# Optimization experiments

Measured on AMD Instinct MI355X. Metric: run time of the kernel, lower is better.

Reference implementation:

```python
import jax, jax.numpy as jnp
import numpy as np

B, N, D, K = 16, 1024, 512, 8
NUM_ITERS = 3
EPS = 1e-08
LN_EPS = 1e-05


def layer_norm(x, g, b):
    m = jnp.mean(x, axis=-1, keepdims=True)
    v = jnp.var(x, axis=-1, keepdims=True)
    return (x - m) * jax.lax.rsqrt(v + LN_EPS) * g + b


def setup_inputs() -> dict:
    key = jax.random.key(0)
    ks = jax.random.split(key, 8)
    s = 1.0 / np.sqrt(D)
    return {
        "embeddings": jax.random.normal(ks[0], (B, N, D), jnp.float32),
        "noise_init": jax.random.normal(ks[1], (B, K, D), jnp.float32),
        "noise_final": jax.random.normal(ks[2], (B, K, D), jnp.float32),
        "slots_mu": jax.random.normal(ks[3], (1, K, D), jnp.float32) * s,
        "slots_logsigma": jax.random.normal(ks[4], (1, K, D), jnp.float32) * s,
        "mixing_coeffs": jnp.ones((1, K), jnp.float32) / K,
        "Wk": jax.random.normal(ks[5], (D, D), jnp.float32) * s,
        "bk": jnp.zeros((D,), jnp.float32),
        "Wq": jax.random.normal(ks[6], (D, D), jnp.float32) * s,
        "bq": jnp.zeros((D,), jnp.float32),
        "Wv": jax.random.normal(ks[7], (D, D), jnp.float32) * s,
        "bv": jnp.zeros((D,), jnp.float32),
        "ln_g": jnp.ones((D,), jnp.float32),
        "ln_b": jnp.zeros((D,), jnp.float32),
    }


def reference(embeddings, noise_init, noise_final, slots_mu, slots_logsigma,
              mixing_coeffs, Wk, bk, Wq, bq, Wv, bv, ln_g, ln_b):
    b, n, d = embeddings.shape
    mixing = jnp.broadcast_to(mixing_coeffs, (b, K))           # [B,K]
    mu = jnp.broadcast_to(slots_mu, (b, K, d))                 # [B,K,D]
    sigma = jnp.exp(jnp.broadcast_to(slots_logsigma, (b, K, d)))
    slots = mu + sigma * noise_init                            # sampled slots

    x = layer_norm(embeddings, ln_g, ln_b)
    keys = x @ Wk + bk                                         # [B,N,D]
    values = x @ Wv + bv                                       # [B,N,D]
    # slots are never updated inside the loop, so queries are loop-invariant
    queries = slots @ Wq + bq                                  # [B,K,D]

    log2pi = jnp.float32(np.log(2.0 * np.pi))
    attn = None
    for _ in range(NUM_ITERS):
        diff = keys[:, :, None, :] - queries[:, None, :, :]    # [B,N,K,D]
        gll = -0.5 * jnp.sum(diff * diff / (sigma[:, None] ** 2 + EPS), axis=-1)  # [B,N,K]
        gll = (-0.5 * d * log2pi
               - 0.5 * jnp.sum(jnp.log(jnp.abs(sigma) + EPS), axis=-1)[:, None, :]
               + gll)
        attn = mixing[:, None, :] * gll                        # [B,N,K]
        attn = attn / jnp.sum(attn, axis=-1, keepdims=True)
        attn = attn / (jnp.sum(attn, axis=1, keepdims=True) + EPS)
        mu = jnp.einsum('bnk,bnd->bkd', attn, values)          # [B,K,D]
        diff2 = values[:, :, None, :] - mu[:, None, :, :]      # [B,N,K,D]
        sigma = jnp.einsum('bnk,bnkd->bkd', attn, diff2 * diff2)
        mixing = jnp.sum(attn, axis=1) / n

    sigma = jnp.maximum(jnp.abs(sigma), EPS)
    slots = mu + sigma * noise_final
    return slots, jnp.transpose(attn, (0, 2, 1))
```

## Files before the change

### kernel.cpp

```cpp
#include <hip/hip_runtime.h>
#include <math.h>

#define BB 16
#define NN 1024
#define DD 512
#define KK 8
#define EPS_ 1e-8f
#define LN_EPS_ 1e-5f
#define GLL_C0 (-470.4965290007924f)

typedef __attribute__((ext_vector_type(8))) short short8;
typedef __attribute__((ext_vector_type(4))) short short4v;
typedef __attribute__((ext_vector_type(4))) float f32x4;
typedef __attribute__((ext_vector_type(4))) int int4v;

static __device__ inline short f2bf(float f) {
    unsigned u = __builtin_bit_cast(unsigned, f);
    u = (u + 0x7fff + ((u >> 16) & 1)) >> 16;
    return (short)u;
}
static __device__ inline float bf2f(short s) {
    unsigned u = ((unsigned)(unsigned short)s) << 16;
    return __builtin_bit_cast(float, u);
}

struct Params {
    const float *emb, *noise_init, *noise_final, *slots_mu, *slots_logsg,
                *mixing_co, *Wk, *bk, *Wq, *bq, *Wv, *bv, *ln_g, *ln_b;
    float *out;
    float *queries, *attn, *s1p, *s2p, *off, *mix16, *colsum;
    short *Abf, *Kbf, *Vbf, *WtKV, *WqT, *slotbf, *F_bt;
};

__global__ __launch_bounds__(256) void k_pre(Params p)
{
    __shared__ __align__(16) short eb[4352];
    int u = blockIdx.x, tid = threadIdx.x;
    if (u < 4096) {
        int row  = u * 4 + (tid >> 6);
        int lane = tid & 63;
        const float* e = p.emb + (size_t)row * DD + lane * 8;
        float4 v0 = *(const float4*)e;
        float4 v1 = *(const float4*)(e + 4);
        float v[8] = {v0.x, v0.y, v0.z, v0.w, v1.x, v1.y, v1.z, v1.w};
        float s = 0.0f;
#pragma unroll
        for (int j = 0; j < 8; j++) s += v[j];
#pragma unroll
        for (int off = 32; off; off >>= 1) s += __shfl_xor(s, off);
        float m = s * (1.0f / DD);
        float vs = 0.0f;
#pragma unroll
        for (int j = 0; j < 8; j++) { float d = v[j] - m; vs = fmaf(d, d, vs); }
#pragma unroll
        for (int off = 32; off; off >>= 1) vs += __shfl_xor(vs, off);
        float rstd = rsqrtf(vs * (1.0f / DD) + LN_EPS_);

        float4 g0 = *(const float4*)&p.ln_g[lane * 8];
        float4 g1 = *(const float4*)&p.ln_g[lane * 8 + 4];
        float4 b0 = *(const float4*)&p.ln_b[lane * 8];
        float4 b1 = *(const float4*)&p.ln_b[lane * 8 + 4];
        float g[8] = {g0.x, g0.y, g0.z, g0.w, g1.x, g1.y, g1.z, g1.w};
        float bb[8] = {b0.x, b0.y, b0.z, b0.w, b1.x, b1.y, b1.z, b1.w};
        short8 o;
#pragma unroll
        for (int j = 0; j < 8; j++) o[j] = f2bf(fmaf((v[j] - m) * rstd, g[j], bb[j]));
        *(short8*)&p.Abf[(size_t)row * DD + lane * 8] = o;
    } else if (u < 4864) {
        int idx = u - 4096;
        int z = idx >> 8, rem = idx & 255;
        const float* W = (z == 0) ? p.Wk : (z == 1) ? p.Wv : p.Wq;
        short* T; int nbase;
        if (z < 2) { T = p.WtKV; nbase = z * 512; } else { T = p.WqT; nbase = 0; }
        int k0 = (rem & 15) * 32, n0 = (rem >> 4) * 32;
        int tx = tid & 31, ty = tid >> 5;
        float (*t)[33] = (float (*)[33])eb;
#pragma unroll
        for (int q = 0; q < 4; q++)
            t[ty + q * 8][tx] = W[(size_t)(k0 + ty + q * 8) * DD + n0 + tx];
        __syncthreads();
#pragma unroll
        for (int q = 0; q < 4; q++)
            T[(size_t)(nbase + n0 + ty + q * 8) * DD + k0 + tx] = f2bf(t[tx][ty + q * 8]);
    } else {
        int idx = u - 4864;
        int b = idx >> 3, k = idx & 7;
#pragma unroll
        for (int q = 0; q < 2; q++) {
            int d = tid + q * 256;
            float sg = expf(p.slots_logsg[k * DD + d]);
            float sl = fmaf(sg, p.noise_init[((size_t)(b * KK + k)) * DD + d],
                            p.slots_mu[k * DD + d]);
            p.slotbf[((size_t)(b * KK + k)) * DD + d] = f2bf(sl);
        }
    }
}

__global__ __launch_bounds__(256) void k_gemm(Params p)
{
    __shared__ __align__(16) short smem[16384];
    int u = blockIdx.x, tid = threadIdx.x;
    int w = tid >> 6, l = tid & 63;
    int x, by, qmode;
    if (u >= 1024) { qmode = 1; x = u - 1024; if (x >= 4) return; by = 128; }
    else           { qmode = 0; x = u >> 7;   by = u & 127; }
    const short* A  = qmode ? p.slotbf : p.Abf + (size_t)by * 128 * DD;
    const short* Bt = qmode ? p.WqT : p.WtKV;
    int row0 = qmode ? 0 : by * 128;
    int col0 = x * 128;

    short* As = smem;
    short* Bs = smem + 8192;
    int sr = l >> 3;
    int sg_off = ((l & 7) ^ sr) * 8;
    int mq = (w & 1) * 64, nq = (w >> 1) * 64;
    int fr = l & 15;
    int orow = (l >> 4) * 4, ocol = l & 15;

    int4v ra[4], rb4[4];
    auto LOADR = [&](int k0) {
#pragma unroll
        for (int j = 0; j < 4; j++) {
            int rbj = w * 32 + j * 8;
            int r   = rbj + sr;
            ra[j]  = *(const int4v*)(A  + (size_t)r * DD + k0 + sg_off);
            rb4[j] = *(const int4v*)(Bt + (size_t)(col0 + r) * DD + k0 + sg_off);
        }
    };
    auto WRITES = [&]() {
#pragma unroll
        for (int j = 0; j < 4; j++) {
            int rbj = w * 32 + j * 8;
            *(int4v*)&As[rbj * 64 + l * 8] = ra[j];
            *(int4v*)&Bs[rbj * 64 + l * 8] = rb4[j];
        }
    };

    f32x4 acc[4][4] = {};
    LOADR(0);
    WRITES();
    __syncthreads();
    for (int i = 0; i < 8; i++) {
        if (i < 7) LOADR((i + 1) * 64);
#pragma unroll
        for (int kk = 0; kk < 2; kk++) {
            int g = kk * 4 + (l >> 4);
            short8 af[4], bfv[4];
#pragma unroll
            for (int mi = 0; mi < 4; mi++)
                af[mi] = *(const short8*)&As[(mq + mi * 16 + fr) * 64 + (g ^ (fr & 7)) * 8];
#pragma unroll
            for (int ni = 0; ni < 4; ni++)
                bfv[ni] = *(const short8*)&Bs[(nq + ni * 16 + fr) * 64 + (g ^ (fr & 7)) * 8];
#pragma unroll
            for (int mi = 0; mi < 4; mi++)
#pragma unroll
                for (int ni = 0; ni < 4; ni++)
                    acc[mi][ni] = __builtin_amdgcn_mfma_f32_16x16x32_bf16(
                        af[mi], bfv[ni], acc[mi][ni], 0, 0, 0);
        }
        __syncthreads();
        if (i < 7) {
            WRITES();
            __syncthreads();
        }
    }

    float bvv[4];
#pragma unroll
    for (int ni = 0; ni < 4; ni++) {
        int col = col0 + nq + ni * 16 + ocol;
        bvv[ni] = qmode ? p.bq[col] : (x < 4 ? p.bk[col] : p.bv[col - 512]);
    }

    if (qmode) {
#pragma unroll
        for (int ni = 0; ni < 4; ni++) {
            int col = col0 + nq + ni * 16 + ocol;
#pragma unroll
            for (int mi = 0; mi < 4; mi++)
#pragma unroll
                for (int r = 0; r < 4; r++)
                    p.queries[(size_t)(mq + mi * 16 + orow + r) * DD + col] =
                        acc[mi][ni][r] + bvv[ni];
        }
    } else {
        short* eb = smem;
        short* dst = (x < 4) ? p.Kbf : p.Vbf;
        int ccol0 = (x & 3) * 128;
#pragma unroll
        for (int mi = 0; mi < 4; mi++)
#pragma unroll
            for (int r = 0; r < 4; r++) {
                int row = mq + mi * 16 + orow + r;
                int sw = ((row >> 2) & 3) << 1;
#pragma unroll
                for (int ni = 0; ni < 4; ni++) {
                    int colg = nq + ni * 16 + ocol;
                    eb[row * 128 + (((colg >> 3) ^ sw) * 8) + (colg & 7)] =
                        f2bf(acc[mi][ni][r] + bvv[ni]);
                }
            }
        __syncthreads();
#pragma unroll
        for (int i = 0; i < 8; i++) {
            int row = i * 16 + w * 4 + (l >> 4);
            int c = l & 15;
            int cc = c ^ (((row >> 2) & 3) << 1);
            short8 vv = *(const short8*)&eb[row * 128 + cc * 8];
            *(short8*)&dst[(size_t)(row0 + row) * 512 + ccol0 + c * 8] = vv;
        }
    }
}

__global__ __launch_bounds__(256) void k_fprep0(Params p)
{
    __shared__ float red[512];
    int u = blockIdx.x, tid = threadIdx.x;
    int b = u >> 4, k = u & 15;
    short* Fr = p.F_bt + (size_t)(b * 16 + k) * 1024;
    if (k >= KK) {
        short4v zv = {0, 0, 0, 0};
        *(short4v*)&Fr[tid * 4] = zv;
        if (tid == 0) { p.off[b * 16 + k] = 0.0f; p.mix16[b * 16 + k] = 0.0f; }
        return;
    }
    float* rc = red;
    float* rl = red + 256;
    float c = 0.0f, ld = 0.0f;
#pragma unroll
    for (int q = 0; q < 2; q++) {
        int d = tid * 2 + q;
        float sg = expf(p.slots_logsg[k * DD + d]);
        float iv = 1.0f / (sg * sg + EPS_);
        float qv = p.queries[((size_t)(b * KK + k)) * DD + d];
        Fr[d]       = f2bf(-0.5f * iv);
        Fr[512 + d] = f2bf(qv * iv);
        c  = fmaf(qv * qv, iv, c);
        ld += logf(fabsf(sg) + EPS_);
    }
    rc[tid] = c; rl[tid] = ld;
    __syncthreads();
    for (int s = 128; s > 0; s >>= 1) {
        if (tid < s) { rc[tid] += rc[tid + s]; rl[tid] += rl[tid + s]; }
        __syncthreads();
    }
    if (tid == 0) {
        p.off[b * 16 + k]    = GLL_C0 - 0.5f * rl[0] - 0.5f * rc[0];
        p.mix16[b * 16 + k]  = p.mixing_co[k];
        p.colsum[b * KK + k] = 0.0f;
    }
}

__global__ __launch_bounds__(512) void k_gllmu(Params p)
{
    __shared__ f32x4 red[3][2][64];
    __shared__ float asml[32 * KK];
    int u = blockIdx.x, tid = threadIdx.x;
    int w = tid >> 6, l = tid & 63;
    int b = u >> 5, chunk = u & 31;
    int n0 = chunk * 32;
    int t = w & 1, ks = w >> 1;

    const short* Ka = p.Kbf + ((size_t)(b * NN + n0 + t * 16 + (l & 15))) * 512
                      + ks * 128 + (l >> 4) * 8;
    const short* Fi = p.F_bt + (size_t)(b * 16 + (l & 15)) * 1024
                      + ks * 128 + (l >> 4) * 8;
    f32x4 acc0 = {}, acc1 = {};
#pragma unroll
    for (int j = 0; j < 4; j++) {
        short8 kf = *(const short8*)&Ka[j * 32];
        short8 f0 = *(const short8*)&Fi[j * 32];
        short8 f1 = *(const short8*)&Fi[j * 32 + 512];
        short8 k2;
#pragma unroll
        for (int e = 0; e < 8; e++) {
            float kv = bf2f(kf[e]);
            k2[e] = f2bf(kv * kv);
        }
        acc0 = __builtin_amdgcn_mfma_f32_16x16x32_bf16(k2, f0, acc0, 0, 0, 0);
        acc1 = __builtin_amdgcn_mfma_f32_16x16x32_bf16(kf, f1, acc1, 0, 0, 0);
    }
    f32x4 acc = acc0 + acc1;

    if (ks) red[ks - 1][t][l] = acc;
    __syncthreads();
    if (ks == 0) {
#pragma unroll
        for (int i = 0; i < 3; i++) acc += red[i][t][l];
        int col = l & 15;
        int rloc = t * 16 + (l >> 4) * 4;
        float offv = p.off[b * 16 + col];
        float mixv = p.mix16[b * 16 + col];
        float a[4], den[4];
#pragma unroll
        for (int r = 0; r < 4; r++) {
            a[r] = mixv * (acc[r] + offv);
            den[r] = a[r];
        }
#pragma unroll
        for (int mask = 1; mask <= 8; mask <<= 1)
#pragma unroll
            for (int r = 0; r < 4; r++) den[r] += __shfl_xor(den[r], mask);
        float csl = 0.0f;
        if (col < KK) {
#pragma unroll
            for (int r = 0; r < 4; r++) {
                float vv = a[r] / den[r];
                asml[(rloc + r) * KK + col] = vv;
                p.attn[((size_t)(b * NN + n0 + rloc + r)) * KK + col] = vv;
                csl += vv;
            }
        }
        csl += __shfl_xor(csl, 16);
        csl += __shfl_xor(csl, 32);
        if (l < KK) atomicAdd(&p.colsum[b * KK + l], csl);
    }
    __syncthreads();

    float s1[KK] = {}, s2[KK] = {};
    const short* vb = p.Vbf + ((size_t)(b * NN + n0)) * DD + tid;
#pragma unroll 4
    for (int nn = 0; nn < 32; nn++) {
        float v = bf2f(vb[(size_t)nn * DD]);
        float vq = v * v;
        float4 a0 = *(const float4*)&asml[nn * KK];
        float4 a1 = *(const float4*)&asml[nn * KK + 4];
        float aa[8] = {a0.x, a0.y, a0.z, a0.w, a1.x, a1.y, a1.z, a1.w};
#pragma unroll
        for (int k = 0; k < KK; k++) {
            s1[k] = fmaf(aa[k], v, s1[k]);
            s2[k] = fmaf(aa[k], vq, s2[k]);
        }
    }
    size_t base = ((size_t)(b * 32 + chunk) * KK) * DD + tid;
#pragma unroll
    for (int k = 0; k < KK; k++) {
        p.s1p[base + (size_t)k * DD] = s1[k];
        p.s2p[base + (size_t)k * DD] = s2[k];
    }
}

__global__ __launch_bounds__(256) void k_fprep(Params p)
{
    __shared__ float red[512];
    int u = blockIdx.x, tid = threadIdx.x;
    int b = u >> 3, k = u & 7;
    float cs   = p.colsum[b * KK + k];
    float inv  = 1.0f / (cs + EPS_);
    float ssum = cs * inv;
    short* Fr = p.F_bt + (size_t)(b * 16 + k) * 1024;
    float* rc = red;
    float* rl = red + 256;
    float c = 0.0f, ld = 0.0f;
#pragma unroll
    for (int q = 0; q < 2; q++) {
        int d = tid * 2 + q;
        float s1 = 0.0f, s2 = 0.0f;
#pragma unroll
        for (int ns = 0; ns < 32; ns++) {
            size_t o = ((size_t)(b * 32 + ns) * KK + k) * DD + d;
            s1 += p.s1p[o];
            s2 += p.s2p[o];
        }
        float m  = s1 * inv;
        float sg = s2 * inv - m * m * (2.0f - ssum);
        float iv = 1.0f / (sg * sg + EPS_);
        float qv = p.queries[((size_t)(b * KK + k)) * DD + d];
        Fr[d]       = f2bf(-0.5f * iv);
        Fr[512 + d] = f2bf(qv * iv);
        c  = fmaf(qv * qv, iv, c);
        ld += logf(fabsf(sg) + EPS_);
    }
    rc[tid] = c; rl[tid] = ld;
    __syncthreads();
    for (int s = 128; s > 0; s >>= 1) {
        if (tid < s) { rc[tid] += rc[tid + s]; rl[tid] += rl[tid + s]; }
        __syncthreads();
    }
    if (tid == 0) {
        p.off[b * 16 + k]    = GLL_C0 - 0.5f * rl[0] - 0.5f * rc[0];
        p.mix16[b * 16 + k]  = ssum * (1.0f / NN);
        p.colsum[b * KK + k] = 0.0f;
    }
}

__global__ __launch_bounds__(256) void k_final(Params p)
{
    int u = blockIdx.x, tid = threadIdx.x;
    if (u < 256) {
        int gid = u * 256 + tid;
        int d = gid & 511;
        int k = (gid >> 9) & 7;
        int b = gid >> 12;
        float s1 = 0.0f, s2 = 0.0f;
#pragma unroll
        for (int ns = 0; ns < 32; ns++) {
            size_t o = ((size_t)(b * 32 + ns) * KK + k) * DD + d;
            s1 += p.s1p[o];
            s2 += p.s2p[o];
        }
        float cs   = p.colsum[b * KK + k];
        float inv  = 1.0f / (cs + EPS_);
        float ssum = cs * inv;
        float m    = s1 * inv;
        float sg   = s2 * inv - m * m * (2.0f - ssum);
        p.out[gid] = fmaf(fmaxf(fabsf(sg), EPS_), p.noise_final[gid], m);
    } else {
        int gid = (u - 256) * 256 + tid;
        int b = gid >> 13;
        int k = (gid >> 10) & 7;
        int n = gid & 1023;
        float cs = p.colsum[b * KK + k];
        p.out[BB * KK * DD + gid] =
            p.attn[((size_t)(b * NN + n)) * KK + k] / (cs + EPS_);
    }
}

extern "C" void kernel_launch(void* const* d_in, const int* in_sizes, int n_in,
                              void* d_out, int out_size, void* d_ws, size_t ws_size,
                              hipStream_t stream)
{
    Params pp;
    pp.emb         = (const float*)d_in[0];
    pp.noise_init  = (const float*)d_in[1];
    pp.noise_final = (const float*)d_in[2];
    pp.slots_mu    = (const float*)d_in[3];
    pp.slots_logsg = (const float*)d_in[4];
    pp.mixing_co   = (const float*)d_in[5];
    pp.Wk          = (const float*)d_in[6];
    pp.bk          = (const float*)d_in[7];
    pp.Wq          = (const float*)d_in[8];
    pp.bq          = (const float*)d_in[9];
    pp.Wv          = (const float*)d_in[10];
    pp.bv          = (const float*)d_in[11];
    pp.ln_g        = (const float*)d_in[12];
    pp.ln_b        = (const float*)d_in[13];
    pp.out         = (float*)d_out;

    float* ws = (float*)d_ws;
    pp.queries = ws;
    pp.attn    = pp.queries + BB * KK * DD;
    pp.s1p     = pp.attn + BB * NN * KK;
    pp.s2p     = pp.s1p + (size_t)BB * 32 * KK * DD;
    pp.off     = pp.s2p + (size_t)BB * 32 * KK * DD;
    pp.mix16   = pp.off + BB * 16;
    pp.colsum  = pp.mix16 + BB * 16;
    pp.Abf     = (short*)(pp.colsum + BB * KK);
    pp.Kbf     = pp.Abf + (size_t)BB * NN * DD;
    pp.Vbf     = pp.Kbf + (size_t)BB * NN * DD;
    pp.WtKV    = pp.Vbf + (size_t)BB * NN * DD;
    pp.WqT     = pp.WtKV + (size_t)1024 * DD;
    pp.slotbf  = pp.WqT + (size_t)DD * DD;
    pp.F_bt    = pp.slotbf + (size_t)BB * KK * DD;

    k_pre<<<4992, 256, 0, stream>>>(pp);
    k_gemm<<<1032, 256, 0, stream>>>(pp);
    k_fprep0<<<256, 256, 0, stream>>>(pp);
    for (int it = 0; it < 3; it++) {
        k_gllmu<<<512, 512, 0, stream>>>(pp);
        if (it < 2) k_fprep<<<128, 256, 0, stream>>>(pp);
    }
    k_final<<<768, 256, 0, stream>>>(pp);
}
```

Baseline: 203.5 us.

## Fuse per-batch reduction and finalize into gllmu via last-block atomic counter

Removes the separate k_fprep and k_final launches. Each k_gllmu block increments a per-batch counter, and the last block to finish for that batch reduces the partial s1/s2 sums and writes either the next iteration's F/off/mix values or the final outputs. Attn is now written only in the last iteration. This cuts kernel-launch gaps but serialises the reduction and finalize work onto just 16 blocks (one per batch), each reducing 8×32×512 partials.

```diff
diff --git a/kernel.cpp b/kernel.cpp
--- a/kernel.cpp
+++ b/kernel.cpp
@@ -29,6 +29,7 @@
                 *mixing_co, *Wk, *bk, *Wq, *bq, *Wv, *bv, *ln_g, *ln_b;
     float *out;
     float *queries, *attn, *s1p, *s2p, *off, *mix16, *colsum;
+    int *cnt;
     short *Abf, *Kbf, *Vbf, *WtKV, *WqT, *slotbf, *F_bt;
 };
 
@@ -218,6 +219,7 @@
     __shared__ float red[512];
     int u = blockIdx.x, tid = threadIdx.x;
     int b = u >> 4, k = u & 15;
+    if (u < 16 && tid == 0) p.cnt[u] = 0;
     short* Fr = p.F_bt + (size_t)(b * 16 + k) * 1024;
     if (k >= KK) {
         short4v zv = {0, 0, 0, 0};
@@ -252,10 +254,12 @@
     }
 }
 
-__global__ __launch_bounds__(512) void k_gllmu(Params p)
+__global__ __launch_bounds__(512) void k_gllmu(Params p, int mode)
 {
     __shared__ f32x4 red[3][2][64];
     __shared__ float asml[32 * KK];
+    __shared__ float redk[2][8][8];
+    __shared__ int lastS;
     int u = blockIdx.x, tid = threadIdx.x;
     int w = tid >> 6, l = tid & 63;
     int b = u >> 5, chunk = u & 31;
@@ -308,7 +312,7 @@
             for (int r = 0; r < 4; r++) {
                 float vv = a[r] / den[r];
                 asml[(rloc + r) * KK + col] = vv;
-                p.attn[((size_t)(b * NN + n0 + rloc + r)) * KK + col] = vv;
+                if (mode) p.attn[((size_t)(b * NN + n0 + rloc + r)) * KK + col] = vv;
                 csl += vv;
             }
         }
@@ -318,102 +322,111 @@
     }
     __syncthreads();
 
-    float s1[KK] = {}, s2[KK] = {};
-    const short* vb = p.Vbf + ((size_t)(b * NN + n0)) * DD + tid;
+    {
+        float s1[KK] = {}, s2[KK] = {};
+        const short* vb = p.Vbf + ((size_t)(b * NN + n0)) * DD + tid;
 #pragma unroll 4
-    for (int nn = 0; nn < 32; nn++) {
-        float v = bf2f(vb[(size_t)nn * DD]);
-        float vq = v * v;
-        float4 a0 = *(const float4*)&asml[nn * KK];
-        float4 a1 = *(const float4*)&asml[nn * KK + 4];
-        float aa[8] = {a0.x, a0.y, a0.z, a0.w, a1.x, a1.y, a1.z, a1.w};
+        for (int nn = 0; nn < 32; nn++) {
+            float v = bf2f(vb[(size_t)nn * DD]);
+            float vq = v * v;
+            float4 a0 = *(const float4*)&asml[nn * KK];
+            float4 a1 = *(const float4*)&asml[nn * KK + 4];
+            float aa[8] = {a0.x, a0.y, a0.z, a0.w, a1.x, a1.y, a1.z, a1.w};
+#pragma unroll
+            for (int k = 0; k < KK; k++) {
+                s1[k] = fmaf(aa[k], v, s1[k]);
+                s2[k] = fmaf(aa[k], vq, s2[k]);
+            }
+        }
+        size_t base = ((size_t)(b * 32 + chunk) * KK) * DD + tid;
 #pragma unroll
         for (int k = 0; k < KK; k++) {
-            s1[k] = fmaf(aa[k], v, s1[k]);
-            s2[k] = fmaf(aa[k], vq, s2[k]);
-        }
-    }
-    size_t base = ((size_t)(b * 32 + chunk) * KK) * DD + tid;
+            p.s1p[base + (size_t)k * DD] = s1[k];
+            p.s2p[base + (size_t)k * DD] = s2[k];
+        }
+    }
+
+    __threadfence();
+    __syncthreads();
+    if (tid == 0) lastS = (atomicAdd(&p.cnt[b], 1) == 31) ? 1 : 0;
+    __syncthreads();
+    if (!lastS) return;
+    __threadfence();
+    if (tid == 0) p.cnt[b] = 0;
+
+    int d = tid;
+    float csv[KK], invv[KK], ssv[KK];
 #pragma unroll
     for (int k = 0; k < KK; k++) {
-        p.s1p[base + (size_t)k * DD] = s1[k];
-        p.s2p[base + (size_t)k * DD] = s2[k];
-    }
-}
-
-__global__ __launch_bounds__(256) void k_fprep(Params p)
-{
-    __shared__ float red[512];
-    int u = blockIdx.x, tid = threadIdx.x;
-    int b = u >> 3, k = u & 7;
-    float cs   = p.colsum[b * KK + k];
-    float inv  = 1.0f / (cs + EPS_);
-    float ssum = cs * inv;
-    short* Fr = p.F_bt + (size_t)(b * 16 + k) * 1024;
-    float* rc = red;
-    float* rl = red + 256;
-    float c = 0.0f, ld = 0.0f;
-#pragma unroll
-    for (int q = 0; q < 2; q++) {
-        int d = tid * 2 + q;
-        float s1 = 0.0f, s2 = 0.0f;
-#pragma unroll
-        for (int ns = 0; ns < 32; ns++) {
-            size_t o = ((size_t)(b * 32 + ns) * KK + k) * DD + d;
-            s1 += p.s1p[o];
-            s2 += p.s2p[o];
-        }
-        float m  = s1 * inv;
-        float sg = s2 * inv - m * m * (2.0f - ssum);
-        float iv = 1.0f / (sg * sg + EPS_);
-        float qv = p.queries[((size_t)(b * KK + k)) * DD + d];
-        Fr[d]       = f2bf(-0.5f * iv);
-        Fr[512 + d] = f2bf(qv * iv);
-        c  = fmaf(qv * qv, iv, c);
-        ld += logf(fabsf(sg) + EPS_);
-    }
-    rc[tid] = c; rl[tid] = ld;
-    __syncthreads();
-    for (int s = 128; s > 0; s >>= 1) {
-        if (tid < s) { rc[tid] += rc[tid + s]; rl[tid] += rl[tid + s]; }
+        csv[k]  = p.colsum[b * KK + k];
+        invv[k] = 1.0f / (csv[k] + EPS_);
+        ssv[k]  = csv[k] * invv[k];
+    }
+
+    if (mode == 0) {
+        float ck[KK], lk[KK];
+#pragma unroll
+        for (int k = 0; k < KK; k++) {
+            float s1 = 0.0f, s2 = 0.0f;
+            for (int ns = 0; ns < 32; ns++) {
+                size_t o = ((size_t)(b * 32 + ns) * KK + k) * DD + d;
+                s1 += p.s1p[o];
+                s2 += p.s2p[o];
+            }
+            float m  = s1 * invv[k];
+            float sg = s2 * invv[k] - m * m * (2.0f - ssv[k]);
+            float iv = 1.0f / (sg * sg + EPS_);
+            float qv = p.queries[((size_t)(b * KK + k)) * DD + d];
+            short* Fr = p.F_bt + (size_t)(b * 16 + k) * 1024;
+            Fr[d]       = f2bf(-0.5f * iv);
+            Fr[512 + d] = f2bf(qv * iv);
+            ck[k] = qv * qv * iv;
+            lk[k] = logf(fabsf(sg) + EPS_);
+        }
+        int wv = tid >> 6, ln = tid & 63;
+#pragma unroll
+        for (int k = 0; k < KK; k++) {
+            float cv = ck[k], lv = lk[k];
+#pragma unroll
+            for (int off = 32; off; off >>= 1) {
+                cv += __shfl_xor(cv, off);
+                lv += __shfl_xor(lv, off);
+            }
+            if (ln == 0) { redk[0][wv][k] = cv; redk[1][wv][k] = lv; }
+        }
         __syncthreads();
-    }
-    if (tid == 0) {
-        p.off[b * 16 + k]    = GLL_C0 - 0.5f * rl[0] - 0.5f * rc[0];
-        p.mix16[b * 16 + k]  = ssum * (1.0f / NN);
-        p.colsum[b * KK + k] = 0.0f;
-    }
-}
-
-__global__ __launch_bounds__(256) void k_final(Params p)
-{
-    int u = blockIdx.x, tid = threadIdx.x;
-    if (u < 256) {
-        int gid = u * 256 + tid;
-        int d = gid & 511;
-        int k = (gid >> 9) & 7;
-        int b = gid >> 12;
-        float s1 = 0.0f, s2 = 0.0f;
-#pragma unroll
-        for (int ns = 0; ns < 32; ns++) {
-            size_t o = ((size_t)(b * 32 + ns) * KK + k) * DD + d;
-            s1 += p.s1p[o];
-            s2 += p.s2p[o];
-        }
-        float cs   = p.colsum[b * KK + k];
-        float inv  = 1.0f / (cs + EPS_);
-        float ssum = cs * inv;
-        float m    = s1 * inv;
-        float sg   = s2 * inv - m * m * (2.0f - ssum);
-        p.out[gid] = fmaf(fmaxf(fabsf(sg), EPS_), p.noise_final[gid], m);
+        if (tid < KK) {
+            float cs_ = 0.0f, ls_ = 0.0f;
+#pragma unroll
+            for (int wv2 = 0; wv2 < 8; wv2++) {
+                cs_ += redk[0][wv2][tid];
+                ls_ += redk[1][wv2][tid];
+            }
+            p.off[b * 16 + tid]    = GLL_C0 - 0.5f * ls_ - 0.5f * cs_;
+            p.mix16[b * 16 + tid]  = ssv[tid] * (1.0f / NN);
+            p.colsum[b * KK + tid] = 0.0f;
+        }
     } else {
-        int gid = (u - 256) * 256 + tid;
-        int b = gid >> 13;
-        int k = (gid >> 10) & 7;
-        int n = gid & 1023;
-        float cs = p.colsum[b * KK + k];
-        p.out[BB * KK * DD + gid] =
-            p.attn[((size_t)(b * NN + n)) * KK + k] / (cs + EPS_);
+#pragma unroll
+        for (int k = 0; k < KK; k++) {
+            float s1 = 0.0f, s2 = 0.0f;
+            for (int ns = 0; ns < 32; ns++) {
+                size_t o = ((size_t)(b * 32 + ns) * KK + k) * DD + d;
+                s1 += p.s1p[o];
+                s2 += p.s2p[o];
+            }
+            float m  = s1 * invv[k];
+            float sg = s2 * invv[k] - m * m * (2.0f - ssv[k]);
+            int gid = (b * KK + k) * DD + d;
+            p.out[gid] = fmaf(fmaxf(fabsf(sg), EPS_), p.noise_final[gid], m);
+        }
+#pragma unroll
+        for (int i = 0; i < 16; i++) {
+            int idx = i * 512 + tid;
+            int k = idx >> 10, n = idx & 1023;
+            p.out[BB * KK * DD + (b * KK + k) * 1024 + n] =
+                p.attn[((size_t)(b * NN + n)) * KK + k] / (csv[k] + EPS_);
+        }
     }
 }
 
@@ -446,7 +459,8 @@
     pp.off     = pp.s2p + (size_t)BB * 32 * KK * DD;
     pp.mix16   = pp.off + BB * 16;
     pp.colsum  = pp.mix16 + BB * 16;
-    pp.Abf     = (short*)(pp.colsum + BB * KK);
+    pp.cnt     = (int*)(pp.colsum + BB * KK);
+    pp.Abf     = (short*)(pp.cnt + 64);
     pp.Kbf     = pp.Abf + (size_t)BB * NN * DD;
     pp.Vbf     = pp.Kbf + (size_t)BB * NN * DD;
     pp.WtKV    = pp.Vbf + (size_t)BB * NN * DD;
@@ -457,9 +471,6 @@
     k_pre<<<4992, 256, 0, stream>>>(pp);
     k_gemm<<<1032, 256, 0, stream>>>(pp);
     k_fprep0<<<256, 256, 0, stream>>>(pp);
-    for (int it = 0; it < 3; it++) {
-        k_gllmu<<<512, 512, 0, stream>>>(pp);
-        if (it < 2) k_fprep<<<128, 256, 0, stream>>>(pp);
-    }
-    k_final<<<768, 256, 0, stream>>>(pp);
-}
+    for (int it = 0; it < 3; it++)
+        k_gllmu<<<512, 512, 0, stream>>>(pp, it == 2 ? 1 : 0);
+}
```

Result: slower. 658.2 us (+223.4%).
